# Kernel optimization log

Hardware: AMD Instinct MI355X
Metric: run time of the kernel (lower is better)

Reference implementation:

```python
import jax, jax.numpy as jnp
import numpy as np

B, PAD_LEN, HID, NB, NY = 1024, 127, 512, 128, 8
IN_DIM = 5 * (PAD_LEN + 1)          # LSTMCell input_size = 5*(pad_len+1)
MAX_TRIP, MAX_ROW = 10, 8
BARGE_PAR_WIDTH = 10.0


def setup_inputs() -> dict:
    key = jax.random.key(0)
    ks = jax.random.split(key, 12)
    s = 1.0 / np.sqrt(HID).astype(np.float32)
    return {
        "x": jax.random.normal(ks[0], (B, IN_DIM), jnp.float32),
        "h0": jnp.zeros((B, HID), jnp.float32),
        "c0": jnp.zeros((B, HID), jnp.float32),
        "W_ih": jax.random.normal(ks[1], (4 * HID, IN_DIM), jnp.float32) * s,
        "W_hh": jax.random.normal(ks[2], (4 * HID, HID), jnp.float32) * s,
        "b_ih": jax.random.normal(ks[3], (4 * HID,), jnp.float32) * s,
        "b_hh": jax.random.normal(ks[4], (4 * HID,), jnp.float32) * s,
        "W_fc": jax.random.normal(ks[5], (NB * NY, HID), jnp.float32) * s,
        "b_fc": jax.random.normal(ks[6], (NB * NY,), jnp.float32) * s,
        "block_size": jax.random.uniform(ks[7], (B, NB, 5), jnp.float32),
        "block_lengths_on_barge": jax.random.uniform(ks[8], (B, NY, MAX_TRIP, MAX_ROW), jnp.float32),
        "block_width_on_barge": jax.random.uniform(ks[9], (B, NY, MAX_TRIP, MAX_ROW), jnp.float32),
        "encoder_mask": jax.random.bernoulli(ks[10], 0.5, (B, NB, NY, PAD_LEN)),
        "block_mask": jnp.zeros((B, NB), bool),
        "barge_count": jax.random.randint(ks[11], (B, NY), 0, MAX_TRIP, jnp.int32),
        "barge_slot": -jnp.ones((B, NY, MAX_TRIP, MAX_ROW, 2), jnp.int32),
    }


def reference(x, h0, c0, W_ih, W_hh, b_ih, b_hh, W_fc, b_fc,
              block_size, block_lengths_on_barge, block_width_on_barge,
              encoder_mask, block_mask, barge_count, barge_slot):
    # ---- LSTMCell step (torch gate order: i, f, g, o) ----
    gates = x @ W_ih.T + b_ih + h0 @ W_hh.T + b_hh          # (B, 4H)
    i, f, g, o = jnp.split(gates, 4, axis=-1)
    c = jax.nn.sigmoid(f) * c0 + jax.nn.sigmoid(i) * jnp.tanh(g)
    h = jax.nn.sigmoid(o) * jnp.tanh(c)

    # ---- fc + masked softmax over (block, yard) joint actions ----
    logits = h @ W_fc.T + b_fc                               # (B, NB*NY)
    yard_feasible = jnp.any(encoder_mask, axis=-1)           # (B, NB, NY): block fits in some slot of yard
    valid = yard_feasible & (~block_mask)[:, :, None]        # unselected blocks only
    neg = jnp.asarray(-1e9, logits.dtype)
    probs = jax.nn.softmax(jnp.where(valid.reshape(valid.shape[0], -1), logits, neg), axis=-1)

    # ---- action decode + per-sample barge-slot scatter allocation ----
    Bsz = x.shape[0]
    bidx = jnp.arange(Bsz)
    action = jnp.argmax(probs, axis=-1)                      # greedy selection
    block_sel = action // NY
    yard_sel = (action % NY).astype(barge_count.dtype)
    cur = barge_count[bidx, yard_sel]                        # (B,) current barge idx per sample
    blen = block_size[bidx, block_sel, 0]                    # (B,)
    bwid = block_size[bidx, block_sel, 1]                    # (B,)

    widths = block_width_on_barge[bidx, yard_sel, cur]       # (B, MAX_ROW) gathered rows
    lens = block_lengths_on_barge[bidx, yard_sel, cur]       # (B, MAX_ROW)
    par_ok = widths <= BARGE_PAR_WIDTH                       # parallel-space feasibility per slot
    cand = jnp.where(par_ok, lens, -1.0)                     # invalid slots -> -1 (as in source)
    slot = jnp.argmax(cand, axis=-1)                         # best existing-length parallel slot

    barge_slot_new = barge_slot.at[bidx, yard_sel, cur, slot, 1].set(block_sel.astype(barge_slot.dtype))
    widths_new = block_width_on_barge.at[bidx, yard_sel, cur, slot].add(bwid)
    lengths_new = block_lengths_on_barge.at[bidx, yard_sel, cur, slot].max(blen)
    return probs, barge_slot_new, lengths_new, widths_new
```

## Files before the change

### kernel.cpp

```cpp
#include <hip/hip_runtime.h>
#include <math.h>

#define Bsz 1024
#define PADL 127
#define HID 512
#define NBb 128
#define NYd 8
#define INDIM 640
#define MTRIP 10
#define MROW 8
#define NBNY 1024
#define FOURH 2048

__device__ __forceinline__ float sigf(float x){ return 1.0f/(1.0f+expf(-x)); }

__global__ __launch_bounds__(256) void yard_kernel(const int* __restrict__ em,
                                                   const int* __restrict__ bmask,
                                                   int* __restrict__ valid)
{
    int r = blockIdx.x*256 + threadIdx.x;
    if (r >= Bsz*NBb*NYd) return;
    const int* p = em + (size_t)r*PADL;
    int any = 0;
    #pragma unroll 1
    for (int j=0; j<PADL; ++j){ if (p[j]!=0){ any=1; break; } }
    int bn = r / NYd;
    valid[r] = (any && (bmask[bn]==0)) ? 1 : 0;
}

__global__ __launch_bounds__(256) void gemm_gates(const float* __restrict__ x,
    const float* __restrict__ h0, const float* __restrict__ Wih,
    const float* __restrict__ Whh, const float* __restrict__ bih,
    const float* __restrict__ bhh, float* __restrict__ gates)
{
    __shared__ float As[16][68];
    __shared__ float Bs[16][68];
    const int tid = threadIdx.x;
    const int m0 = blockIdx.y*64, n0 = blockIdx.x*64;
    const int lm = tid>>2, lk = (tid&3)*4;
    const int tm = (tid>>4)*4, tn = (tid&15)*4;
    float acc[4][4] = {{0.f,0.f,0.f,0.f},{0.f,0.f,0.f,0.f},{0.f,0.f,0.f,0.f},{0.f,0.f,0.f,0.f}};

    {
        const float* Arow = x   + (m0+lm)*INDIM + lk;
        const float* Brow = Wih + (n0+lm)*INDIM + lk;
        for (int k0=0; k0<INDIM; k0+=16){
            float4 av = *(const float4*)(Arow + k0);
            float4 bv = *(const float4*)(Brow + k0);
            As[lk+0][lm]=av.x; As[lk+1][lm]=av.y; As[lk+2][lm]=av.z; As[lk+3][lm]=av.w;
            Bs[lk+0][lm]=bv.x; Bs[lk+1][lm]=bv.y; Bs[lk+2][lm]=bv.z; Bs[lk+3][lm]=bv.w;
            __syncthreads();
            #pragma unroll
            for (int kk=0; kk<16; ++kk){
                float4 a = *(const float4*)&As[kk][tm];
                float4 b = *(const float4*)&Bs[kk][tn];
                float a4[4]={a.x,a.y,a.z,a.w}, b4[4]={b.x,b.y,b.z,b.w};
                #pragma unroll
                for (int i=0;i<4;i++)
                    #pragma unroll
                    for (int j=0;j<4;j++) acc[i][j] += a4[i]*b4[j];
            }
            __syncthreads();
        }
    }
    {
        const float* Arow = h0  + (m0+lm)*HID + lk;
        const float* Brow = Whh + (n0+lm)*HID + lk;
        for (int k0=0; k0<HID; k0+=16){
            float4 av = *(const float4*)(Arow + k0);
            float4 bv = *(const float4*)(Brow + k0);
            As[lk+0][lm]=av.x; As[lk+1][lm]=av.y; As[lk+2][lm]=av.z; As[lk+3][lm]=av.w;
            Bs[lk+0][lm]=bv.x; Bs[lk+1][lm]=bv.y; Bs[lk+2][lm]=bv.z; Bs[lk+3][lm]=bv.w;
            __syncthreads();
            #pragma unroll
            for (int kk=0; kk<16; ++kk){
                float4 a = *(const float4*)&As[kk][tm];
                float4 b = *(const float4*)&Bs[kk][tn];
                float a4[4]={a.x,a.y,a.z,a.w}, b4[4]={b.x,b.y,b.z,b.w};
                #pragma unroll
                for (int i=0;i<4;i++)
                    #pragma unroll
                    for (int j=0;j<4;j++) acc[i][j] += a4[i]*b4[j];
            }
            __syncthreads();
        }
    }
    #pragma unroll
    for (int i=0;i<4;i++){
        int row = m0+tm+i;
        #pragma unroll
        for (int j=0;j<4;j++){
            int col = n0+tn+j;
            gates[row*FOURH + col] = acc[i][j] + bih[col] + bhh[col];
        }
    }
}

__global__ __launch_bounds__(256) void gemm_fc(const float* __restrict__ h,
    const float* __restrict__ Wfc, const float* __restrict__ bfc,
    float* __restrict__ logits)
{
    __shared__ float As[16][68];
    __shared__ float Bs[16][68];
    const int tid = threadIdx.x;
    const int m0 = blockIdx.y*64, n0 = blockIdx.x*64;
    const int lm = tid>>2, lk = (tid&3)*4;
    const int tm = (tid>>4)*4, tn = (tid&15)*4;
    float acc[4][4] = {{0.f,0.f,0.f,0.f},{0.f,0.f,0.f,0.f},{0.f,0.f,0.f,0.f},{0.f,0.f,0.f,0.f}};

    const float* Arow = h   + (m0+lm)*HID + lk;
    const float* Brow = Wfc + (n0+lm)*HID + lk;
    for (int k0=0; k0<HID; k0+=16){
        float4 av = *(const float4*)(Arow + k0);
        float4 bv = *(const float4*)(Brow + k0);
        As[lk+0][lm]=av.x; As[lk+1][lm]=av.y; As[lk+2][lm]=av.z; As[lk+3][lm]=av.w;
        Bs[lk+0][lm]=bv.x; Bs[lk+1][lm]=bv.y; Bs[lk+2][lm]=bv.z; Bs[lk+3][lm]=bv.w;
        __syncthreads();
        #pragma unroll
        for (int kk=0; kk<16; ++kk){
            float4 a = *(const float4*)&As[kk][tm];
            float4 b = *(const float4*)&Bs[kk][tn];
            float a4[4]={a.x,a.y,a.z,a.w}, b4[4]={b.x,b.y,b.z,b.w};
            #pragma unroll
            for (int i=0;i<4;i++)
                #pragma unroll
                for (int j=0;j<4;j++) acc[i][j] += a4[i]*b4[j];
        }
        __syncthreads();
    }
    #pragma unroll
    for (int i=0;i<4;i++){
        int row = m0+tm+i;
        #pragma unroll
        for (int j=0;j<4;j++){
            int col = n0+tn+j;
            logits[row*NBNY + col] = acc[i][j] + bfc[col];
        }
    }
}

__global__ __launch_bounds__(256) void lstm_kernel(const float* __restrict__ gates,
    const float* __restrict__ c0, float* __restrict__ h)
{
    int idx = blockIdx.x*256 + threadIdx.x;
    int b = idx >> 9, j = idx & 511;
    const float* g = gates + b*FOURH;
    float ig = g[j], fg = g[512+j], gg = g[1024+j], og = g[1536+j];
    float c = sigf(fg)*c0[idx] + sigf(ig)*tanhf(gg);
    h[idx] = sigf(og)*tanhf(c);
}

__global__ __launch_bounds__(256) void softmax_kernel(const float* __restrict__ logits,
    const int* __restrict__ valid, float* __restrict__ probs, int* __restrict__ action)
{
    int b = blockIdx.x, t = threadIdx.x;
    __shared__ float red[256];
    __shared__ int  redi[256];
    const float* lrow = logits + b*NBNY;
    const int*   vrow = valid  + b*NBNY;
    float ml[4]; float mymax = -INFINITY;
    #pragma unroll
    for (int r=0;r<4;++r){
        int c = t + r*256;
        float m = (vrow[c]!=0) ? lrow[c] : -1e9f;
        ml[r] = m; mymax = fmaxf(mymax, m);
    }
    red[t]=mymax; __syncthreads();
    for (int s=128;s>0;s>>=1){ if(t<s) red[t]=fmaxf(red[t],red[t+s]); __syncthreads(); }
    float rowmax = red[0]; __syncthreads();
    float p[4]; float mysum=0.f;
    #pragma unroll
    for (int r=0;r<4;++r){ p[r]=expf(ml[r]-rowmax); mysum+=p[r]; }
    red[t]=mysum; __syncthreads();
    for (int s=128;s>0;s>>=1){ if(t<s) red[t]+=red[t+s]; __syncthreads(); }
    float inv = 1.0f/red[0]; __syncthreads();
    float bv=-INFINITY; int bi=0;
    #pragma unroll
    for (int r=0;r<4;++r){
        int c = t + r*256;
        float pr = p[r]*inv;
        probs[b*NBNY + c] = pr;
        if (pr > bv){ bv=pr; bi=c; }
    }
    red[t]=bv; redi[t]=bi; __syncthreads();
    for (int s=128;s>0;s>>=1){
        if (t<s){
            float ov=red[t+s]; int oi=redi[t+s];
            if (ov>red[t] || (ov==red[t] && oi<redi[t])){ red[t]=ov; redi[t]=oi; }
        }
        __syncthreads();
    }
    if (t==0) action[b]=redi[0];
}

__global__ __launch_bounds__(256) void decode_kernel(const int* __restrict__ action,
    const int* __restrict__ bcount, const float* __restrict__ bsize,
    const float* __restrict__ bwid_in, const float* __restrict__ blen_in,
    int* __restrict__ pslot, int* __restrict__ pblock,
    float* __restrict__ pblen, float* __restrict__ pbwid)
{
    int b = blockIdx.x*256 + threadIdx.x;
    if (b >= Bsz) return;
    int a = action[b];
    int blk = a / NYd, yard = a % NYd;
    int cur = bcount[b*NYd + yard];
    int base = ((b*NYd + yard)*MTRIP + cur)*MROW;
    float bestv = -INFINITY; int bests = 0;
    #pragma unroll
    for (int s=0;s<MROW;++s){
        float w = bwid_in[base+s];
        float l = blen_in[base+s];
        float cand = (w <= 10.0f) ? l : -1.0f;
        if (cand > bestv){ bestv=cand; bests=s; }
    }
    pslot[b]  = base + bests;
    pblock[b] = blk;
    pblen[b]  = bsize[(b*NBb + blk)*5 + 0];
    pbwid[b]  = bsize[(b*NBb + blk)*5 + 1];
}

__global__ __launch_bounds__(256) void finalize_kernel(const int* __restrict__ bslot,
    const float* __restrict__ blen_in, const float* __restrict__ bwid_in,
    const int* __restrict__ pslot, const int* __restrict__ pblock,
    const float* __restrict__ pblen, const float* __restrict__ pbwid,
    float* __restrict__ out_slot, float* __restrict__ out_len, float* __restrict__ out_wid)
{
    int i = blockIdx.x*256 + threadIdx.x;
    if (i < Bsz*NYd*MTRIP*MROW*2){
        int b = i / (NYd*MTRIP*MROW*2);
        float v = (float)bslot[i];
        if (i == pslot[b]*2 + 1) v = (float)pblock[b];
        out_slot[i] = v;
    }
    if (i < Bsz*NYd*MTRIP*MROW){
        int b = i / (NYd*MTRIP*MROW);
        float l = blen_in[i], w = bwid_in[i];
        if (i == pslot[b]){ l = fmaxf(l, pblen[b]); w = w + pbwid[b]; }
        out_len[i] = l;
        out_wid[i] = w;
    }
}

extern "C" void kernel_launch(void* const* d_in, const int* in_sizes, int n_in,
                              void* d_out, int out_size, void* d_ws, size_t ws_size,
                              hipStream_t stream)
{
    const float* x    = (const float*)d_in[0];
    const float* h0   = (const float*)d_in[1];
    const float* c0   = (const float*)d_in[2];
    const float* Wih  = (const float*)d_in[3];
    const float* Whh  = (const float*)d_in[4];
    const float* bih  = (const float*)d_in[5];
    const float* bhh  = (const float*)d_in[6];
    const float* Wfc  = (const float*)d_in[7];
    const float* bfc  = (const float*)d_in[8];
    const float* bsize= (const float*)d_in[9];
    const float* blen = (const float*)d_in[10];
    const float* bwid = (const float*)d_in[11];
    const int*   em   = (const int*)d_in[12];
    const int*   bmask= (const int*)d_in[13];
    const int*   bcount=(const int*)d_in[14];
    const int*   bslot= (const int*)d_in[15];

    float* out      = (float*)d_out;
    float* probs    = out;
    float* out_slot = out + 1048576;
    float* out_len  = out + 1048576 + 1310720;
    float* out_wid  = out_len + 655360;

    float* ws     = (float*)d_ws;
    float* gates  = ws;
    float* h      = ws + 2097152;
    float* logits = ws + 2621440;
    int*   valid  = (int*)(ws + 3670016);
    int*   action = (int*)(ws + 4718592);
    int*   pslot  = (int*)(ws + 4719616);
    int*   pblock = (int*)(ws + 4720640);
    float* pblen  = ws + 4721664;
    float* pbwid  = ws + 4722688;

    yard_kernel<<<4096, 256, 0, stream>>>(em, bmask, valid);
    gemm_gates<<<dim3(32,16), 256, 0, stream>>>(x, h0, Wih, Whh, bih, bhh, gates);
    lstm_kernel<<<2048, 256, 0, stream>>>(gates, c0, h);
    gemm_fc<<<dim3(16,16), 256, 0, stream>>>(h, Wfc, bfc, logits);
    softmax_kernel<<<1024, 256, 0, stream>>>(logits, valid, probs, action);
    decode_kernel<<<4, 256, 0, stream>>>(action, bcount, bsize, bwid, blen,
                                         pslot, pblock, pblen, pbwid);
    finalize_kernel<<<5120, 256, 0, stream>>>(bslot, blen, bwid, pslot, pblock, pblen, pbwid,
                                              out_slot, out_len, out_wid);
}
```

Before: 782.0 us.

## Fuse mask scan and decode into softmax, double-buffer and retile GEMMs, vectorize LSTM

The encoder-mask any-reduction now runs inside the softmax kernel, and the greedy decode runs in that kernel's thread 0, which removes the yard and decode kernels and the valid/action buffers. Both GEMMs share one templated kernel with register prefetch and double-buffered shared memory. The gates GEMM uses 128-row tiles and loops over both K segments in one pipeline. The LSTM cell step uses float4 loads and stores. The mask scan is now done by only 256 threads per row over long strided rows, which may reduce memory parallelism for the dominant encoder-mask read.

```diff
diff --git a/kernel.cpp b/kernel.cpp
--- a/kernel.cpp
+++ b/kernel.cpp
@@ -14,127 +14,89 @@
 
 __device__ __forceinline__ float sigf(float x){ return 1.0f/(1.0f+expf(-x)); }
 
-__global__ __launch_bounds__(256) void yard_kernel(const int* __restrict__ em,
-                                                   const int* __restrict__ bmask,
-                                                   int* __restrict__ valid)
-{
-    int r = blockIdx.x*256 + threadIdx.x;
-    if (r >= Bsz*NBb*NYd) return;
-    const int* p = em + (size_t)r*PADL;
-    int any = 0;
-    #pragma unroll 1
-    for (int j=0; j<PADL; ++j){ if (p[j]!=0){ any=1; break; } }
-    int bn = r / NYd;
-    valid[r] = (any && (bmask[bn]==0)) ? 1 : 0;
-}
-
-__global__ __launch_bounds__(256) void gemm_gates(const float* __restrict__ x,
-    const float* __restrict__ h0, const float* __restrict__ Wih,
-    const float* __restrict__ Whh, const float* __restrict__ bih,
-    const float* __restrict__ bhh, float* __restrict__ gates)
-{
-    __shared__ float As[16][68];
-    __shared__ float Bs[16][68];
+template<int TM>
+__global__ __launch_bounds__(256) void gemm_bias(
+    const float* __restrict__ A1, const float* __restrict__ B1, int K1,
+    const float* __restrict__ A2, const float* __restrict__ B2, int K2,
+    const float* __restrict__ bias1, const float* __restrict__ bias2,
+    float* __restrict__ C, int ldc)
+{
+    constexpr int BM = TM*16;
+    __shared__ float As[2][16][BM+4];
+    __shared__ float Bs[2][16][68];
     const int tid = threadIdx.x;
-    const int m0 = blockIdx.y*64, n0 = blockIdx.x*64;
-    const int lm = tid>>2, lk = (tid&3)*4;
-    const int tm = (tid>>4)*4, tn = (tid&15)*4;
-    float acc[4][4] = {{0.f,0.f,0.f,0.f},{0.f,0.f,0.f,0.f},{0.f,0.f,0.f,0.f},{0.f,0.f,0.f,0.f}};
-
-    {
-        const float* Arow = x   + (m0+lm)*INDIM + lk;
-        const float* Brow = Wih + (n0+lm)*INDIM + lk;
-        for (int k0=0; k0<INDIM; k0+=16){
-            float4 av = *(const float4*)(Arow + k0);
-            float4 bv = *(const float4*)(Brow + k0);
-            As[lk+0][lm]=av.x; As[lk+1][lm]=av.y; As[lk+2][lm]=av.z; As[lk+3][lm]=av.w;
-            Bs[lk+0][lm]=bv.x; Bs[lk+1][lm]=bv.y; Bs[lk+2][lm]=bv.z; Bs[lk+3][lm]=bv.w;
+    const int m0 = blockIdx.y*BM, n0 = blockIdx.x*64;
+
+    const int ar = (TM==8) ? (tid>>1) : (tid>>2);
+    const int ac = (TM==8) ? ((tid&1)*8) : ((tid&3)*4);
+    const int br = tid>>2, bc = (tid&3)*4;
+
+    const int tm = (tid>>4)*TM, tn = (tid&15)*4;
+
+    float acc[TM][4];
+    #pragma unroll
+    for (int i=0;i<TM;i++){
+        #pragma unroll
+        for (int j=0;j<4;j++) acc[i][j]=0.f;
+    }
+
+    const int P1 = K1/16;
+    const int nsteps = P1 + K2/16;
+
+    float4 pa0, pa1, pb0;
+    auto prefetch = [&](int s){
+        const float* A; const float* B; int K; int k0;
+        if (s < P1){ A=A1; B=B1; K=K1; k0 = s*16; }
+        else       { A=A2; B=B2; K=K2; k0 = (s-P1)*16; }
+        const float* ap = A + (size_t)(m0+ar)*K + k0 + ac;
+        pa0 = *(const float4*)ap;
+        if (TM==8) pa1 = *(const float4*)(ap+4);
+        pb0 = *(const float4*)(B + (size_t)(n0+br)*K + k0 + bc);
+    };
+    auto stage = [&](int buf){
+        As[buf][ac+0][ar]=pa0.x; As[buf][ac+1][ar]=pa0.y;
+        As[buf][ac+2][ar]=pa0.z; As[buf][ac+3][ar]=pa0.w;
+        if (TM==8){
+            As[buf][ac+4][ar]=pa1.x; As[buf][ac+5][ar]=pa1.y;
+            As[buf][ac+6][ar]=pa1.z; As[buf][ac+7][ar]=pa1.w;
+        }
+        Bs[buf][bc+0][br]=pb0.x; Bs[buf][bc+1][br]=pb0.y;
+        Bs[buf][bc+2][br]=pb0.z; Bs[buf][bc+3][br]=pb0.w;
+    };
+
+    prefetch(0);
+    stage(0);
+    __syncthreads();
+    int buf = 0;
+    for (int s=0; s<nsteps; ++s){
+        if (s+1 < nsteps) prefetch(s+1);
+        #pragma unroll
+        for (int kk=0; kk<16; ++kk){
+            float a[TM], b[4];
+            #pragma unroll
+            for (int i=0;i<TM;i++) a[i] = As[buf][kk][tm+i];
+            #pragma unroll
+            for (int j=0;j<4;j++)  b[j] = Bs[buf][kk][tn+j];
+            #pragma unroll
+            for (int i=0;i<TM;i++)
+                #pragma unroll
+                for (int j=0;j<4;j++) acc[i][j] += a[i]*b[j];
+        }
+        if (s+1 < nsteps){
+            stage(buf^1);
             __syncthreads();
-            #pragma unroll
-            for (int kk=0; kk<16; ++kk){
-                float4 a = *(const float4*)&As[kk][tm];
-                float4 b = *(const float4*)&Bs[kk][tn];
-                float a4[4]={a.x,a.y,a.z,a.w}, b4[4]={b.x,b.y,b.z,b.w};
-                #pragma unroll
-                for (int i=0;i<4;i++)
-                    #pragma unroll
-                    for (int j=0;j<4;j++) acc[i][j] += a4[i]*b4[j];
-            }
-            __syncthreads();
-        }
-    }
-    {
-        const float* Arow = h0  + (m0+lm)*HID + lk;
-        const float* Brow = Whh + (n0+lm)*HID + lk;
-        for (int k0=0; k0<HID; k0+=16){
-            float4 av = *(const float4*)(Arow + k0);
-            float4 bv = *(const float4*)(Brow + k0);
-            As[lk+0][lm]=av.x; As[lk+1][lm]=av.y; As[lk+2][lm]=av.z; As[lk+3][lm]=av.w;
-            Bs[lk+0][lm]=bv.x; Bs[lk+1][lm]=bv.y; Bs[lk+2][lm]=bv.z; Bs[lk+3][lm]=bv.w;
-            __syncthreads();
-            #pragma unroll
-            for (int kk=0; kk<16; ++kk){
-                float4 a = *(const float4*)&As[kk][tm];
-                float4 b = *(const float4*)&Bs[kk][tn];
-                float a4[4]={a.x,a.y,a.z,a.w}, b4[4]={b.x,b.y,b.z,b.w};
-                #pragma unroll
-                for (int i=0;i<4;i++)
-                    #pragma unroll
-                    for (int j=0;j<4;j++) acc[i][j] += a4[i]*b4[j];
-            }
-            __syncthreads();
-        }
-    }
-    #pragma unroll
-    for (int i=0;i<4;i++){
+            buf ^= 1;
+        }
+    }
+
+    #pragma unroll
+    for (int i=0;i<TM;i++){
         int row = m0+tm+i;
         #pragma unroll
         for (int j=0;j<4;j++){
             int col = n0+tn+j;
-            gates[row*FOURH + col] = acc[i][j] + bih[col] + bhh[col];
-        }
-    }
-}
-
-__global__ __launch_bounds__(256) void gemm_fc(const float* __restrict__ h,
-    const float* __restrict__ Wfc, const float* __restrict__ bfc,
-    float* __restrict__ logits)
-{
-    __shared__ float As[16][68];
-    __shared__ float Bs[16][68];
-    const int tid = threadIdx.x;
-    const int m0 = blockIdx.y*64, n0 = blockIdx.x*64;
-    const int lm = tid>>2, lk = (tid&3)*4;
-    const int tm = (tid>>4)*4, tn = (tid&15)*4;
-    float acc[4][4] = {{0.f,0.f,0.f,0.f},{0.f,0.f,0.f,0.f},{0.f,0.f,0.f,0.f},{0.f,0.f,0.f,0.f}};
-
-    const float* Arow = h   + (m0+lm)*HID + lk;
-    const float* Brow = Wfc + (n0+lm)*HID + lk;
-    for (int k0=0; k0<HID; k0+=16){
-        float4 av = *(const float4*)(Arow + k0);
-        float4 bv = *(const float4*)(Brow + k0);
-        As[lk+0][lm]=av.x; As[lk+1][lm]=av.y; As[lk+2][lm]=av.z; As[lk+3][lm]=av.w;
-        Bs[lk+0][lm]=bv.x; Bs[lk+1][lm]=bv.y; Bs[lk+2][lm]=bv.z; Bs[lk+3][lm]=bv.w;
-        __syncthreads();
-        #pragma unroll
-        for (int kk=0; kk<16; ++kk){
-            float4 a = *(const float4*)&As[kk][tm];
-            float4 b = *(const float4*)&Bs[kk][tn];
-            float a4[4]={a.x,a.y,a.z,a.w}, b4[4]={b.x,b.y,b.z,b.w};
-            #pragma unroll
-            for (int i=0;i<4;i++)
-                #pragma unroll
-                for (int j=0;j<4;j++) acc[i][j] += a4[i]*b4[j];
-        }
-        __syncthreads();
-    }
-    #pragma unroll
-    for (int i=0;i<4;i++){
-        int row = m0+tm+i;
-        #pragma unroll
-        for (int j=0;j<4;j++){
-            int col = n0+tn+j;
-            logits[row*NBNY + col] = acc[i][j] + bfc[col];
+            float bsum = bias1[col] + (bias2 ? bias2[col] : 0.f);
+            C[(size_t)row*ldc + col] = acc[i][j] + bsum;
         }
     }
 }
@@ -143,43 +105,71 @@
     const float* __restrict__ c0, float* __restrict__ h)
 {
     int idx = blockIdx.x*256 + threadIdx.x;
-    int b = idx >> 9, j = idx & 511;
-    const float* g = gates + b*FOURH;
-    float ig = g[j], fg = g[512+j], gg = g[1024+j], og = g[1536+j];
-    float c = sigf(fg)*c0[idx] + sigf(ig)*tanhf(gg);
-    h[idx] = sigf(og)*tanhf(c);
-}
-
-__global__ __launch_bounds__(256) void softmax_kernel(const float* __restrict__ logits,
-    const int* __restrict__ valid, float* __restrict__ probs, int* __restrict__ action)
+    int b = idx >> 7, j4 = (idx & 127)*4;
+    const float* g = gates + (size_t)b*FOURH;
+    float4 iv = *(const float4*)(g + j4);
+    float4 fv = *(const float4*)(g + 512 + j4);
+    float4 gv = *(const float4*)(g + 1024 + j4);
+    float4 ov = *(const float4*)(g + 1536 + j4);
+    float4 cv = *(const float4*)(c0 + (size_t)b*HID + j4);
+    float4 hv;
+    hv.x = sigf(ov.x)*tanhf(sigf(fv.x)*cv.x + sigf(iv.x)*tanhf(gv.x));
+    hv.y = sigf(ov.y)*tanhf(sigf(fv.y)*cv.y + sigf(iv.y)*tanhf(gv.y));
+    hv.z = sigf(ov.z)*tanhf(sigf(fv.z)*cv.z + sigf(iv.z)*tanhf(gv.z));
+    hv.w = sigf(ov.w)*tanhf(sigf(fv.w)*cv.w + sigf(iv.w)*tanhf(gv.w));
+    *(float4*)(h + (size_t)b*HID + j4) = hv;
+}
+
+__device__ __forceinline__ int row_any(const int* __restrict__ p){
+    #pragma unroll 1
+    for (int j=0; j<124; j+=4){
+        if (p[j] | p[j+1] | p[j+2] | p[j+3]) return 1;
+    }
+    return (p[124] | p[125] | p[126]) ? 1 : 0;
+}
+
+__global__ __launch_bounds__(256) void softmax_fused(
+    const float* __restrict__ logits, const int* __restrict__ em,
+    const int* __restrict__ bmask, const int* __restrict__ bcount,
+    const float* __restrict__ bsize, const float* __restrict__ bwid_in,
+    const float* __restrict__ blen_in,
+    float* __restrict__ probs,
+    int* __restrict__ pslot, int* __restrict__ pblock,
+    float* __restrict__ pblen, float* __restrict__ pbwid)
 {
     int b = blockIdx.x, t = threadIdx.x;
     __shared__ float red[256];
     __shared__ int  redi[256];
-    const float* lrow = logits + b*NBNY;
-    const int*   vrow = valid  + b*NBNY;
+    const float* lrow = logits + (size_t)b*NBNY;
+
     float ml[4]; float mymax = -INFINITY;
     #pragma unroll
     for (int r=0;r<4;++r){
         int c = t + r*256;
-        float m = (vrow[c]!=0) ? lrow[c] : -1e9f;
+        int nb = c >> 3;
+        int v = 0;
+        if (bmask[b*NBb + nb] == 0)
+            v = row_any(em + (size_t)(b*NBNY + c)*PADL);
+        float m = v ? lrow[c] : -1e9f;
         ml[r] = m; mymax = fmaxf(mymax, m);
     }
     red[t]=mymax; __syncthreads();
     for (int s=128;s>0;s>>=1){ if(t<s) red[t]=fmaxf(red[t],red[t+s]); __syncthreads(); }
     float rowmax = red[0]; __syncthreads();
+
     float p[4]; float mysum=0.f;
     #pragma unroll
     for (int r=0;r<4;++r){ p[r]=expf(ml[r]-rowmax); mysum+=p[r]; }
     red[t]=mysum; __syncthreads();
     for (int s=128;s>0;s>>=1){ if(t<s) red[t]+=red[t+s]; __syncthreads(); }
     float inv = 1.0f/red[0]; __syncthreads();
+
     float bv=-INFINITY; int bi=0;
     #pragma unroll
     for (int r=0;r<4;++r){
         int c = t + r*256;
         float pr = p[r]*inv;
-        probs[b*NBNY + c] = pr;
+        probs[(size_t)b*NBNY + c] = pr;
         if (pr > bv){ bv=pr; bi=c; }
     }
     red[t]=bv; redi[t]=bi; __syncthreads();
@@ -190,33 +180,25 @@
         }
         __syncthreads();
     }
-    if (t==0) action[b]=redi[0];
-}
-
-__global__ __launch_bounds__(256) void decode_kernel(const int* __restrict__ action,
-    const int* __restrict__ bcount, const float* __restrict__ bsize,
-    const float* __restrict__ bwid_in, const float* __restrict__ blen_in,
-    int* __restrict__ pslot, int* __restrict__ pblock,
-    float* __restrict__ pblen, float* __restrict__ pbwid)
-{
-    int b = blockIdx.x*256 + threadIdx.x;
-    if (b >= Bsz) return;
-    int a = action[b];
-    int blk = a / NYd, yard = a % NYd;
-    int cur = bcount[b*NYd + yard];
-    int base = ((b*NYd + yard)*MTRIP + cur)*MROW;
-    float bestv = -INFINITY; int bests = 0;
-    #pragma unroll
-    for (int s=0;s<MROW;++s){
-        float w = bwid_in[base+s];
-        float l = blen_in[base+s];
-        float cand = (w <= 10.0f) ? l : -1.0f;
-        if (cand > bestv){ bestv=cand; bests=s; }
-    }
-    pslot[b]  = base + bests;
-    pblock[b] = blk;
-    pblen[b]  = bsize[(b*NBb + blk)*5 + 0];
-    pbwid[b]  = bsize[(b*NBb + blk)*5 + 1];
+
+    if (t==0){
+        int a = redi[0];
+        int blk = a / NYd, yard = a % NYd;
+        int cur = bcount[b*NYd + yard];
+        int base = ((b*NYd + yard)*MTRIP + cur)*MROW;
+        float bestv = -INFINITY; int bests = 0;
+        #pragma unroll
+        for (int s=0;s<MROW;++s){
+            float w = bwid_in[base+s];
+            float l = blen_in[base+s];
+            float cand = (w <= 10.0f) ? l : -1.0f;
+            if (cand > bestv){ bestv=cand; bests=s; }
+        }
+        pslot[b]  = base + bests;
+        pblock[b] = blk;
+        pblen[b]  = bsize[(b*NBb + blk)*5 + 0];
+        pbwid[b]  = bsize[(b*NBb + blk)*5 + 1];
+    }
 }
 
 __global__ __launch_bounds__(256) void finalize_kernel(const int* __restrict__ bslot,
@@ -272,20 +254,18 @@
     float* gates  = ws;
     float* h      = ws + 2097152;
     float* logits = ws + 2621440;
-    int*   valid  = (int*)(ws + 3670016);
-    int*   action = (int*)(ws + 4718592);
-    int*   pslot  = (int*)(ws + 4719616);
-    int*   pblock = (int*)(ws + 4720640);
-    float* pblen  = ws + 4721664;
-    float* pbwid  = ws + 4722688;
-
-    yard_kernel<<<4096, 256, 0, stream>>>(em, bmask, valid);
-    gemm_gates<<<dim3(32,16), 256, 0, stream>>>(x, h0, Wih, Whh, bih, bhh, gates);
-    lstm_kernel<<<2048, 256, 0, stream>>>(gates, c0, h);
-    gemm_fc<<<dim3(16,16), 256, 0, stream>>>(h, Wfc, bfc, logits);
-    softmax_kernel<<<1024, 256, 0, stream>>>(logits, valid, probs, action);
-    decode_kernel<<<4, 256, 0, stream>>>(action, bcount, bsize, bwid, blen,
-                                         pslot, pblock, pblen, pbwid);
+    int*   pslot  = (int*)(ws + 3670016);
+    int*   pblock = (int*)(ws + 3671040);
+    float* pblen  = ws + 3672064;
+    float* pbwid  = ws + 3673088;
+
+    gemm_bias<8><<<dim3(FOURH/64, Bsz/128), 256, 0, stream>>>(
+        x, Wih, INDIM, h0, Whh, HID, bih, bhh, gates, FOURH);
+    lstm_kernel<<<512, 256, 0, stream>>>(gates, c0, h);
+    gemm_bias<4><<<dim3(NBNY/64, Bsz/64), 256, 0, stream>>>(
+        h, Wfc, HID, nullptr, nullptr, 0, bfc, nullptr, logits, NBNY);
+    softmax_fused<<<Bsz, 256, 0, stream>>>(logits, em, bmask, bcount, bsize, bwid, blen,
+                                           probs, pslot, pblock, pblen, pbwid);
     finalize_kernel<<<5120, 256, 0, stream>>>(bslot, blen, bwid, pslot, pblock, pblen, pbwid,
                                               out_slot, out_len, out_wid);
 }
```

Result: slower. 810.0 us (+3.6%).
